# Optimization experiments

Measured on AMD Instinct MI355X. Metric: run time of the kernel, lower is better.

The kernel has to match this reference:

```python
import jax, jax.numpy as jnp
import numpy as np

NUM_HEADS = 8


def setup_inputs() -> dict:
    key = jax.random.key(0)
    k1, k2, k3 = jax.random.split(key, 3)
    B, L, E, H = 4, 2048, 256, NUM_HEADS
    x = jax.random.normal(k1, (B, L, E), dtype=jnp.float32)
    W_qkv = jax.random.normal(k2, (E, H * E * 3), dtype=jnp.float32) * 0.02
    W_out = jax.random.normal(k3, (H * E, E), dtype=jnp.float32) * 0.02
    return {"x": x, "W_qkv": W_qkv, "W_out": W_out}


def reference(x, W_qkv, W_out):
    B, L, E = x.shape
    H = NUM_HEADS
    qkv = x @ W_qkv  # [B, L, 3*H*E]
    q, k, v = jnp.split(qkv, 3, axis=-1)  # each [B, L, H*E]
    # reshape(B, L, H, E) then move heads before sequence -> [B, H, L, E]
    q = q.reshape(B, L, H, E).transpose(0, 2, 1, 3)
    k = k.reshape(B, L, H, E).transpose(0, 2, 1, 3)
    v = v.reshape(B, L, H, E).transpose(0, 2, 1, 3)
    scale = 1.0 / jnp.sqrt(jnp.asarray(E, dtype=x.dtype))
    scores = jnp.einsum("bhqe,bhke->bhqk", q, k) * scale  # [B, H, L, L]
    attn = jax.nn.softmax(scores, axis=-1)
    out = jnp.einsum("bhqk,bhke->bhqe", attn, v)  # [B, H, L, E]
    out = out.transpose(0, 2, 1, 3).reshape(B, L, H * E)
    return out @ W_out  # [B, L, E]
```

## Files before the change

### kernel.cpp

```cpp
#include <hip/hip_runtime.h>
#include <cstdint>
#include <cstddef>

typedef __bf16 bf16_t;
typedef __bf16 bf16x8 __attribute__((ext_vector_type(8)));
typedef __bf16 bf16x4 __attribute__((ext_vector_type(4)));
typedef float  f32x4  __attribute__((ext_vector_type(4)));
typedef int    i32x4  __attribute__((ext_vector_type(4)));

#define MFMA16(a, b, c) __builtin_amdgcn_mfma_f32_16x16x32_bf16((a), (b), (c), 0, 0, 0)

__device__ __forceinline__ void gload_lds16(const bf16_t* g, bf16_t* l) {
  __builtin_amdgcn_global_load_lds(
      (__attribute__((address_space(1))) void*)((void*)g),
      (__attribute__((address_space(3))) void*)l, 16, 0, 0);
}

__global__ __launch_bounds__(256) void cvt_f32_bf16(
    const float* __restrict__ in, bf16_t* __restrict__ out, int n) {
  const int i = (blockIdx.x * 256 + threadIdx.x) * 4;
  if (i + 3 < n) {
    const float4 v = *(const float4*)(in + i);
    bf16x4 o;
    o[0] = (bf16_t)v.x; o[1] = (bf16_t)v.y; o[2] = (bf16_t)v.z; o[3] = (bf16_t)v.w;
    *(bf16x4*)(out + i) = o;
  }
}

__global__ __launch_bounds__(256) void transpose_f32_bf16(
    const float* __restrict__ in, bf16_t* __restrict__ out, int R, int C) {
  __shared__ bf16_t tile[32][33];
  const int bc = blockIdx.x * 32, br = blockIdx.y * 32;
  const int tx = threadIdx.x, ty = threadIdx.y;
#pragma unroll
  for (int i = 0; i < 32; i += 8)
    tile[ty + i][tx] = (bf16_t)in[(size_t)(br + ty + i) * C + bc + tx];
  __syncthreads();
#pragma unroll
  for (int i = 0; i < 32; i += 8)
    out[(size_t)(bc + ty + i) * R + br + tx] = tile[tx][ty + i];
}

template <int EPI>
__global__ __launch_bounds__(256) void gemm_bt(
    const bf16_t* __restrict__ A, const bf16_t* __restrict__ Bt,
    void* __restrict__ Cout, bf16_t* __restrict__ Vt, int M, int N, int K) {
  __shared__ __align__(16) bf16_t As[128 * 32];
  __shared__ __align__(16) bf16_t Bs[128 * 32];
  const int tid = threadIdx.x;
  const int lane = tid & 63, w = tid >> 6;
  const int wm = w >> 1, wn = w & 1;
  const int bm = blockIdx.y * 128, bn = blockIdx.x * 128;
  const int l15 = lane & 15, l4 = lane >> 4;

  f32x4 acc[4][4] = {};

  for (int k0 = 0; k0 < K; k0 += 32) {
    __syncthreads();
#pragma unroll
    for (int i = 0; i < 2; ++i) {
      const int idx = i * 256 + tid;
      const int r = idx >> 2, s = idx & 3;
      const int ss = s ^ (r & 3);
      gload_lds16(A + (size_t)(bm + r) * K + k0 + ss * 8, &As[idx * 8]);
      gload_lds16(Bt + (size_t)(bn + r) * K + k0 + ss * 8, &Bs[idx * 8]);
    }
    __syncthreads();
    bf16x8 af[4], bfr[4];
#pragma unroll
    for (int f = 0; f < 4; ++f) {
      const int ra = wm * 64 + f * 16 + l15;
      const int rb = wn * 64 + f * 16 + l15;
      af[f]  = *(const bf16x8*)&As[ra * 32 + (l4 ^ (ra & 3)) * 8];
      bfr[f] = *(const bf16x8*)&Bs[rb * 32 + (l4 ^ (rb & 3)) * 8];
    }
#pragma unroll
    for (int i = 0; i < 4; ++i)
#pragma unroll
      for (int j = 0; j < 4; ++j) acc[i][j] = MFMA16(af[i], bfr[j], acc[i][j]);
  }

#pragma unroll
  for (int i = 0; i < 4; ++i) {
    const int gr = bm + wm * 64 + i * 16 + l4 * 4;
#pragma unroll
    for (int j = 0; j < 4; ++j) {
      const int gc = bn + wn * 64 + j * 16 + l15;
      if constexpr (EPI == 0) {
        float* C = (float*)Cout;
#pragma unroll
        for (int r = 0; r < 4; ++r)
          C[(size_t)(gr + r) * N + gc] = acc[i][j][r];
      } else {
        bf16_t* C = (bf16_t*)Cout;
        if (gc < 4096) {
#pragma unroll
          for (int r = 0; r < 4; ++r)
            C[(size_t)(gr + r) * 4096 + gc] = (bf16_t)acc[i][j][r];
        } else {
          const int c = gc - 4096, h = c >> 8, d = c & 255;
          const int b = gr >> 11, lt = gr & 2047;
          bf16x4 pk;
#pragma unroll
          for (int r = 0; r < 4; ++r) pk[r] = (bf16_t)acc[i][j][r];
          *(bf16x4*)&Vt[((size_t)(b * 8 + h) * 256 + d) * 2048 + lt] = pk;
        }
      }
    }
  }
}

__global__ __launch_bounds__(512, 2) void attn_fwd(
    const bf16_t* __restrict__ qk, const bf16_t* __restrict__ vt,
    bf16_t* __restrict__ ao) {
  __shared__ __align__(16) bf16_t Ks[64 * 256];
  __shared__ __align__(16) bf16_t Vs[256 * 64];
  __shared__ __align__(16) bf16_t Ps[8][16 * 72];
  const int tid = threadIdx.x, lane = tid & 63, w = tid >> 6;
  const int l15 = lane & 15, l4 = lane >> 4;
  const int bid = blockIdx.x;
  const int swz = (bid & 7) * 64 + (bid >> 3);
  const int qb = swz & 15;
  const int bh = swz >> 4;
  const int b = bh >> 3, h = bh & 7;
  const float scale = 0.0625f;

  const int qrow = qb * 128 + w * 16 + l15;
  const bf16_t* qbase =
      qk + (size_t)(b * 2048 + qrow) * 4096 + h * 256 + l4 * 8;
  bf16x8 qf[8];
#pragma unroll
  for (int kk = 0; kk < 8; ++kk) qf[kk] = *(const bf16x8*)(qbase + kk * 32);

  const bf16_t* kg = qk + (size_t)(b * 2048) * 4096 + 2048 + h * 256;
  const bf16_t* vg = vt + (size_t)bh * 256 * 2048;

  int krow[4], kseg[4], vrow[4], vseg[4];
#pragma unroll
  for (int i = 0; i < 4; ++i) {
    const int idx = i * 512 + tid;
    krow[i] = idx >> 5; kseg[i] = idx & 31;
    vrow[i] = idx >> 3; vseg[i] = idx & 7;
  }

  i32x4 stK[4], stV[4];
#pragma unroll
  for (int i = 0; i < 4; ++i) {
    stK[i] = *(const i32x4*)(kg + (size_t)krow[i] * 4096 + kseg[i] * 8);
    stV[i] = *(const i32x4*)(vg + (size_t)vrow[i] * 2048 + vseg[i] * 8);
  }

  f32x4 o[16] = {};
  float m = -1e30f, lsum = 0.f;

  for (int kv = 0; kv < 32; ++kv) {
    __syncthreads();
#pragma unroll
    for (int i = 0; i < 4; ++i) {
      *(i32x4*)&Ks[(krow[i] * 32 + (kseg[i] ^ (krow[i] & 7))) * 8] = stK[i];
      *(i32x4*)&Vs[(vrow[i] * 8 + (vseg[i] ^ (vrow[i] & 7))) * 8] = stV[i];
    }
    __syncthreads();
    const int nx = (kv + 1 < 32) ? kv + 1 : kv;
#pragma unroll
    for (int i = 0; i < 4; ++i) {
      stK[i] = *(const i32x4*)(kg + (size_t)(nx * 64 + krow[i]) * 4096 + kseg[i] * 8);
      stV[i] = *(const i32x4*)(vg + (size_t)vrow[i] * 2048 + nx * 64 + vseg[i] * 8);
    }

    f32x4 s4[4] = {};
    __builtin_amdgcn_s_setprio(1);
#pragma unroll
    for (int kk = 0; kk < 8; ++kk) {
#pragma unroll
      for (int fn = 0; fn < 4; ++fn) {
        bf16x8 kf = *(const bf16x8*)
            &Ks[((fn * 16 + l15) * 32 + ((kk * 4 + l4) ^ (l15 & 7))) * 8];
        s4[fn] = MFMA16(kf, qf[kk], s4[fn]);
      }
    }
    __builtin_amdgcn_s_setprio(0);

    float v = s4[0][0];
#pragma unroll
    for (int fn = 0; fn < 4; ++fn)
#pragma unroll
      for (int r = 0; r < 4; ++r) v = fmaxf(v, s4[fn][r]);
    v = fmaxf(v, __shfl_xor(v, 16));
    v = fmaxf(v, __shfl_xor(v, 32));
    const float mn = fmaxf(m, v * scale);
    const float al = __expf(m - mn);
    m = mn;

    float rs = 0.f;
#pragma unroll
    for (int fn = 0; fn < 4; ++fn) {
      bf16x4 pw;
#pragma unroll
      for (int r = 0; r < 4; ++r) {
        const float p = __expf(s4[fn][r] * scale - mn);
        rs += p;
        pw[r] = (bf16_t)p;
      }
      *(bf16x4*)&Ps[w][l15 * 72 + fn * 16 + l4 * 4] = pw;
    }
    rs += __shfl_xor(rs, 16);
    rs += __shfl_xor(rs, 32);
    lsum = lsum * al + rs;
#pragma unroll
    for (int fd = 0; fd < 16; ++fd) {
      o[fd][0] *= al; o[fd][1] *= al; o[fd][2] *= al; o[fd][3] *= al;
    }

    bf16x8 pb[2];
#pragma unroll
    for (int ks = 0; ks < 2; ++ks)
      pb[ks] = *(const bf16x8*)&Ps[w][l15 * 72 + ks * 32 + l4 * 8];
    __builtin_amdgcn_s_setprio(1);
#pragma unroll
    for (int ks = 0; ks < 2; ++ks) {
#pragma unroll
      for (int fd = 0; fd < 16; ++fd) {
        bf16x8 vf = *(const bf16x8*)
            &Vs[((fd * 16 + l15) * 8 + ((ks * 4 + l4) ^ (l15 & 7))) * 8];
        o[fd] = MFMA16(vf, pb[ks], o[fd]);
      }
    }
    __builtin_amdgcn_s_setprio(0);
  }

  const float inv = 1.0f / lsum;
#pragma unroll
  for (int fd = 0; fd < 16; ++fd) {
    bf16x4 ov;
#pragma unroll
    for (int r = 0; r < 4; ++r) ov[r] = (bf16_t)(o[fd][r] * inv);
    *(bf16x4*)&ao[(size_t)(b * 2048 + qrow) * 2048 + h * 256 + fd * 16 + l4 * 4] = ov;
  }
}

extern "C" void kernel_launch(void* const* d_in, const int* in_sizes, int n_in,
                              void* d_out, int out_size, void* d_ws,
                              size_t ws_size, hipStream_t stream) {
  (void)in_sizes; (void)n_in; (void)out_size; (void)ws_size;
  const float* x    = (const float*)d_in[0];
  const float* wqkv = (const float*)d_in[1];
  const float* wout = (const float*)d_in[2];
  float* out = (float*)d_out;

  char* ws = (char*)d_ws;
  bf16_t* xb  = (bf16_t*)(ws);
  bf16_t* wqt = (bf16_t*)(ws + 4194304);
  bf16_t* wot = (bf16_t*)(ws + 7340032);
  bf16_t* qkb = (bf16_t*)(ws + 8388608);
  bf16_t* vtb = (bf16_t*)(ws + 8388608 + 67108864);
  bf16_t* aob = (bf16_t*)(ws + 8388608 + 67108864 + 33554432);

  cvt_f32_bf16<<<2048, 256, 0, stream>>>(x, xb, 8192 * 256);
  transpose_f32_bf16<<<dim3(192, 8), dim3(32, 8), 0, stream>>>(wqkv, wqt, 256, 6144);
  transpose_f32_bf16<<<dim3(8, 64), dim3(32, 8), 0, stream>>>(wout, wot, 2048, 256);
  gemm_bt<1><<<dim3(48, 64), 256, 0, stream>>>(xb, wqt, qkb, vtb, 8192, 6144, 256);
  attn_fwd<<<512, 512, 0, stream>>>(qkb, vtb, aob);
  gemm_bt<0><<<dim3(2, 64), 256, 0, stream>>>(aob, wot, out, nullptr, 8192, 256, 2048);
}
```

Baseline: 295.9 us.

## Rewrite attention with 32x32 MFMA, register-resident P, and double-buffered async K/V

Switches attention to 32x32x16 MFMA tiles with 256-query blocks, halving the grid. P is kept in registers using cvt_pk and permlane32_swap rather than a round trip through LDS. K/V tiles are double-buffered and loaded straight into LDS with global_load_lds, synchronised by waitcnt and barriers. The softmax scale is folded into the Q GEMM epilogue, and the output rescale is skipped when the running max does not change. The risks are higher register pressure (128 accumulator floats plus 16 Q fragments per lane), 128 KB of LDS per block, and reduced occupancy with only 256 blocks.

```diff
diff --git a/kernel.cpp b/kernel.cpp
--- a/kernel.cpp
+++ b/kernel.cpp
@@ -6,9 +6,14 @@
 typedef __bf16 bf16x8 __attribute__((ext_vector_type(8)));
 typedef __bf16 bf16x4 __attribute__((ext_vector_type(4)));
 typedef float  f32x4  __attribute__((ext_vector_type(4)));
-typedef int    i32x4  __attribute__((ext_vector_type(4)));
+typedef float  f32x16 __attribute__((ext_vector_type(16)));
 
 #define MFMA16(a, b, c) __builtin_amdgcn_mfma_f32_16x16x32_bf16((a), (b), (c), 0, 0, 0)
+#define MFMA32(a, b, c) __builtin_amdgcn_mfma_f32_32x32x16_bf16((a), (b), (c), 0, 0, 0)
+#define CVTPK(d, a, b) \
+  asm("v_cvt_pk_bf16_f32 %0, %1, %2" : "=v"(d) : "v"(a), "v"(b))
+#define PLSWAP(a, b) \
+  asm("v_permlane32_swap_b32 %0, %1" : "+v"(a), "+v"(b))
 
 __device__ __forceinline__ void gload_lds16(const bf16_t* g, bf16_t* l) {
   __builtin_amdgcn_global_load_lds(
@@ -93,7 +98,11 @@
           C[(size_t)(gr + r) * N + gc] = acc[i][j][r];
       } else {
         bf16_t* C = (bf16_t*)Cout;
-        if (gc < 4096) {
+        if (gc < 2048) {
+#pragma unroll
+          for (int r = 0; r < 4; ++r)
+            C[(size_t)(gr + r) * 4096 + gc] = (bf16_t)(acc[i][j][r] * 0.0625f);
+        } else if (gc < 4096) {
 #pragma unroll
           for (int r = 0; r < 4; ++r)
             C[(size_t)(gr + r) * 4096 + gc] = (bf16_t)acc[i][j][r];
@@ -113,130 +122,134 @@
 __global__ __launch_bounds__(512, 2) void attn_fwd(
     const bf16_t* __restrict__ qk, const bf16_t* __restrict__ vt,
     bf16_t* __restrict__ ao) {
-  __shared__ __align__(16) bf16_t Ks[64 * 256];
-  __shared__ __align__(16) bf16_t Vs[256 * 64];
-  __shared__ __align__(16) bf16_t Ps[8][16 * 72];
+  __shared__ __align__(16) bf16_t Ks[2][64 * 256];
+  __shared__ __align__(16) bf16_t Vs[2][256 * 64];
   const int tid = threadIdx.x, lane = tid & 63, w = tid >> 6;
-  const int l15 = lane & 15, l4 = lane >> 4;
+  const int l31 = lane & 31, h5 = lane >> 5, p3 = l31 & 7;
   const int bid = blockIdx.x;
-  const int swz = (bid & 7) * 64 + (bid >> 3);
-  const int qb = swz & 15;
-  const int bh = swz >> 4;
-  const int b = bh >> 3, h = bh & 7;
-  const float scale = 0.0625f;
-
-  const int qrow = qb * 128 + w * 16 + l15;
+  const int swz = (bid & 7) * 32 + (bid >> 3);
+  const int qt = swz & 7;
+  const int bh = swz >> 3;
+  const int bb = bh >> 3, hh = bh & 7;
+
+  const int qcol = qt * 256 + w * 32 + l31;
   const bf16_t* qbase =
-      qk + (size_t)(b * 2048 + qrow) * 4096 + h * 256 + l4 * 8;
-  bf16x8 qf[8];
-#pragma unroll
-  for (int kk = 0; kk < 8; ++kk) qf[kk] = *(const bf16x8*)(qbase + kk * 32);
-
-  const bf16_t* kg = qk + (size_t)(b * 2048) * 4096 + 2048 + h * 256;
+      qk + (size_t)(bb * 2048 + qcol) * 4096 + hh * 256 + h5 * 8;
+  bf16x8 qf[16];
+#pragma unroll
+  for (int s = 0; s < 16; ++s) qf[s] = *(const bf16x8*)(qbase + s * 16);
+
+  const bf16_t* kg = qk + (size_t)(bb * 2048) * 4096 + 2048 + hh * 256;
   const bf16_t* vg = vt + (size_t)bh * 256 * 2048;
 
-  int krow[4], kseg[4], vrow[4], vseg[4];
-#pragma unroll
-  for (int i = 0; i < 4; ++i) {
-    const int idx = i * 512 + tid;
-    krow[i] = idx >> 5; kseg[i] = idx & 31;
-    vrow[i] = idx >> 3; vseg[i] = idx & 7;
-  }
-
-  i32x4 stK[4], stV[4];
-#pragma unroll
-  for (int i = 0; i < 4; ++i) {
-    stK[i] = *(const i32x4*)(kg + (size_t)krow[i] * 4096 + kseg[i] * 8);
-    stV[i] = *(const i32x4*)(vg + (size_t)vrow[i] * 2048 + vseg[i] * 8);
-  }
-
-  f32x4 o[16] = {};
+#define STAGE_TILES(bufidx, tile)                                           \
+  {                                                                         \
+    const int t64 = (tile) * 64;                                            \
+    _Pragma("unroll") for (int c = 0; c < 4; ++c) {                         \
+      const int idx = c * 512 + tid;                                        \
+      const int kr = idx >> 5, kse = idx & 31;                              \
+      gload_lds16(kg + (size_t)(t64 + kr) * 4096 + ((kse ^ (kr & 7)) * 8),  \
+                  &Ks[bufidx][idx * 8]);                                    \
+    }                                                                       \
+    _Pragma("unroll") for (int c = 0; c < 4; ++c) {                         \
+      const int idx = c * 512 + tid;                                        \
+      const int vr = idx >> 3, vse = idx & 7;                               \
+      gload_lds16(vg + (size_t)vr * 2048 + t64 + ((vse ^ (vr & 7)) * 8),    \
+                  &Vs[bufidx][idx * 8]);                                    \
+    }                                                                       \
+  }
+
+  STAGE_TILES(0, 0);
+  STAGE_TILES(1, 1);
+
+  f32x16 o[8] = {};
   float m = -1e30f, lsum = 0.f;
 
   for (int kv = 0; kv < 32; ++kv) {
-    __syncthreads();
-#pragma unroll
-    for (int i = 0; i < 4; ++i) {
-      *(i32x4*)&Ks[(krow[i] * 32 + (kseg[i] ^ (krow[i] & 7))) * 8] = stK[i];
-      *(i32x4*)&Vs[(vrow[i] * 8 + (vseg[i] ^ (vrow[i] & 7))) * 8] = stV[i];
-    }
-    __syncthreads();
-    const int nx = (kv + 1 < 32) ? kv + 1 : kv;
-#pragma unroll
-    for (int i = 0; i < 4; ++i) {
-      stK[i] = *(const i32x4*)(kg + (size_t)(nx * 64 + krow[i]) * 4096 + kseg[i] * 8);
-      stV[i] = *(const i32x4*)(vg + (size_t)vrow[i] * 2048 + nx * 64 + vseg[i] * 8);
-    }
-
-    f32x4 s4[4] = {};
+    const int cur = kv & 1;
+    asm volatile("s_waitcnt vmcnt(8)" ::: "memory");
+    __builtin_amdgcn_s_barrier();
+    __builtin_amdgcn_sched_barrier(0);
+    const bf16_t* Kc = Ks[cur];
+    const bf16_t* Vc = Vs[cur];
+
+    f32x16 sa0 = {}, sa1 = {};
     __builtin_amdgcn_s_setprio(1);
 #pragma unroll
-    for (int kk = 0; kk < 8; ++kk) {
-#pragma unroll
-      for (int fn = 0; fn < 4; ++fn) {
-        bf16x8 kf = *(const bf16x8*)
-            &Ks[((fn * 16 + l15) * 32 + ((kk * 4 + l4) ^ (l15 & 7))) * 8];
-        s4[fn] = MFMA16(kf, qf[kk], s4[fn]);
-      }
+    for (int s = 0; s < 16; ++s) {
+      const int so = ((2 * s + h5) ^ p3) << 4;
+      bf16x8 kf0 = *(const bf16x8*)((const char*)Kc + l31 * 512 + so);
+      bf16x8 kf1 = *(const bf16x8*)((const char*)Kc + (32 + l31) * 512 + so);
+      sa0 = MFMA32(kf0, qf[s], sa0);
+      sa1 = MFMA32(kf1, qf[s], sa1);
     }
     __builtin_amdgcn_s_setprio(0);
 
-    float v = s4[0][0];
-#pragma unroll
-    for (int fn = 0; fn < 4; ++fn)
-#pragma unroll
-      for (int r = 0; r < 4; ++r) v = fmaxf(v, s4[fn][r]);
-    v = fmaxf(v, __shfl_xor(v, 16));
-    v = fmaxf(v, __shfl_xor(v, 32));
-    const float mn = fmaxf(m, v * scale);
-    const float al = __expf(m - mn);
-    m = mn;
-
+    float pm = sa0[0];
+#pragma unroll
+    for (int r = 1; r < 16; ++r) pm = fmaxf(pm, sa0[r]);
+#pragma unroll
+    for (int r = 0; r < 16; ++r) pm = fmaxf(pm, sa1[r]);
+    pm = fmaxf(pm, __shfl_xor(pm, 32));
+    if (!__all(pm <= m)) {
+      const float mn = fmaxf(m, pm);
+      const float al = __expf(m - mn);
+      m = mn;
+      lsum *= al;
+#pragma unroll
+      for (int dt = 0; dt < 8; ++dt)
+#pragma unroll
+        for (int r = 0; r < 16; ++r) o[dt][r] *= al;
+    }
     float rs = 0.f;
 #pragma unroll
-    for (int fn = 0; fn < 4; ++fn) {
-      bf16x4 pw;
-#pragma unroll
-      for (int r = 0; r < 4; ++r) {
-        const float p = __expf(s4[fn][r] * scale - mn);
-        rs += p;
-        pw[r] = (bf16_t)p;
-      }
-      *(bf16x4*)&Ps[w][l15 * 72 + fn * 16 + l4 * 4] = pw;
-    }
-    rs += __shfl_xor(rs, 16);
+    for (int r = 0; r < 16; ++r) { sa0[r] = __expf(sa0[r] - m); rs += sa0[r]; }
+#pragma unroll
+    for (int r = 0; r < 16; ++r) { sa1[r] = __expf(sa1[r] - m); rs += sa1[r]; }
     rs += __shfl_xor(rs, 32);
-    lsum = lsum * al + rs;
-#pragma unroll
-    for (int fd = 0; fd < 16; ++fd) {
-      o[fd][0] *= al; o[fd][1] *= al; o[fd][2] *= al; o[fd][3] *= al;
-    }
-
-    bf16x8 pb[2];
-#pragma unroll
-    for (int ks = 0; ks < 2; ++ks)
-      pb[ks] = *(const bf16x8*)&Ps[w][l15 * 72 + ks * 32 + l4 * 8];
+    lsum += rs;
+
     __builtin_amdgcn_s_setprio(1);
-#pragma unroll
-    for (int ks = 0; ks < 2; ++ks) {
-#pragma unroll
-      for (int fd = 0; fd < 16; ++fd) {
-        bf16x8 vf = *(const bf16x8*)
-            &Vs[((fd * 16 + l15) * 8 + ((ks * 4 + l4) ^ (l15 & 7))) * 8];
-        o[fd] = MFMA16(vf, pb[ks], o[fd]);
-      }
-    }
+#define PV_KSTEP(SA, c0, s2)                                                \
+    {                                                                       \
+      unsigned w0, w1, w2, w3;                                              \
+      CVTPK(w0, SA[4 * (c0) + 0], SA[4 * (c0) + 1]);                        \
+      CVTPK(w2, SA[4 * (c0) + 4], SA[4 * (c0) + 5]);                        \
+      PLSWAP(w0, w2);                                                       \
+      CVTPK(w1, SA[4 * (c0) + 2], SA[4 * (c0) + 3]);                        \
+      CVTPK(w3, SA[4 * (c0) + 6], SA[4 * (c0) + 7]);                        \
+      PLSWAP(w1, w3);                                                       \
+      union { unsigned u[4]; bf16x8 v; } pu;                                \
+      pu.u[0] = w0; pu.u[1] = w1; pu.u[2] = w2; pu.u[3] = w3;               \
+      _Pragma("unroll") for (int dt = 0; dt < 8; ++dt) {                    \
+        bf16x8 vf = *(const bf16x8*)((const char*)Vc +                      \
+            (dt * 32 + l31) * 128 + (((2 * (s2) + h5) ^ p3) << 4));         \
+        o[dt] = MFMA32(vf, pu.v, o[dt]);                                    \
+      }                                                                     \
+    }
+    PV_KSTEP(sa0, 0, 0);
+    PV_KSTEP(sa0, 2, 1);
+    PV_KSTEP(sa1, 0, 2);
+    PV_KSTEP(sa1, 2, 3);
     __builtin_amdgcn_s_setprio(0);
+
+    __builtin_amdgcn_sched_barrier(0);
+    __builtin_amdgcn_s_barrier();
+    __builtin_amdgcn_sched_barrier(0);
+    STAGE_TILES(cur, (kv + 2) & 31);
   }
 
   const float inv = 1.0f / lsum;
-#pragma unroll
-  for (int fd = 0; fd < 16; ++fd) {
-    bf16x4 ov;
-#pragma unroll
-    for (int r = 0; r < 4; ++r) ov[r] = (bf16_t)(o[fd][r] * inv);
-    *(bf16x4*)&ao[(size_t)(b * 2048 + qrow) * 2048 + h * 256 + fd * 16 + l4 * 4] = ov;
-  }
+  bf16_t* aor = ao + (size_t)(bb * 2048 + qcol) * 2048 + hh * 256 + 4 * h5;
+#pragma unroll
+  for (int dt = 0; dt < 8; ++dt)
+#pragma unroll
+    for (int c = 0; c < 4; ++c) {
+      bf16x4 ov;
+#pragma unroll
+      for (int bq = 0; bq < 4; ++bq) ov[bq] = (bf16_t)(o[dt][4 * c + bq] * inv);
+      *(bf16x4*)(aor + dt * 32 + 8 * c) = ov;
+    }
 }
 
 extern "C" void kernel_launch(void* const* d_in, const int* in_sizes, int n_in,
@@ -260,6 +273,6 @@
   transpose_f32_bf16<<<dim3(192, 8), dim3(32, 8), 0, stream>>>(wqkv, wqt, 256, 6144);
   transpose_f32_bf16<<<dim3(8, 64), dim3(32, 8), 0, stream>>>(wout, wot, 2048, 256);
   gemm_bt<1><<<dim3(48, 64), 256, 0, stream>>>(xb, wqt, qkb, vtb, 8192, 6144, 256);
-  attn_fwd<<<512, 512, 0, stream>>>(qkb, vtb, aob);
+  attn_fwd<<<256, 512, 0, stream>>>(qkb, vtb, aob);
   gemm_bt<0><<<dim3(2, 64), 256, 0, stream>>>(aob, wot, out, nullptr, 8192, 256, 2048);
 }
```

Result: slower. 571.6 us (+93.2%).
